# Kernel optimization log

Hardware: AMD Instinct MI355X
Metric: run time of the kernel (lower is better)

The kernel has to match this reference:

```python
import jax, jax.numpy as jnp
import numpy as np

N, K, D = 524288, 32, 8
EPS = 1e-6


def setup_inputs() -> dict:
    key = jax.random.key(0)
    k1, k2, k3, k4 = jax.random.split(key, 4)
    x = jax.random.normal(k1, (N, D), dtype=jnp.float32)
    pi = jax.random.uniform(k2, (K,), dtype=jnp.float32)
    means = jax.random.normal(k3, (K, D), dtype=jnp.float32)
    # eye + small perturbation keeps tril(chol_var) well-conditioned (PD covariance)
    chol_var = jnp.eye(D, dtype=jnp.float32)[None] + 0.1 * jax.random.normal(k4, (K, D, D), dtype=jnp.float32)
    return {"x": x, "pi": pi, "means": means, "chol_var": chol_var}


def reference(x, pi, means, chol_var):
    d = x.shape[-1]
    L = jnp.tril(chol_var)                                   # [K,d,d]
    cov = jnp.einsum('kij,klj->kil', L, L) + EPS * jnp.eye(d, dtype=x.dtype)
    C = jnp.linalg.cholesky(cov)                             # [K,d,d] (MVN recomputes cholesky)
    logdet = 2.0 * jnp.sum(jnp.log(jnp.diagonal(C, axis1=-2, axis2=-1)), axis=-1)  # [K]
    eye = jnp.eye(d, dtype=x.dtype)
    Cinv = jax.vmap(lambda c: jax.scipy.linalg.solve_triangular(c, eye, lower=True))(C)  # [K,d,d]
    zx = jnp.einsum('kij,nj->nki', Cinv, x)                  # [N,K,d]
    zm = jnp.einsum('kij,kj->ki', Cinv, means)               # [K,d]
    maha = jnp.sum((zx - zm[None]) ** 2, axis=-1)            # [N,K]
    log_2pi = jnp.log(2.0 * jnp.pi).astype(x.dtype)
    log_probs = -0.5 * (maha + d * log_2pi + logdet[None])   # [N,K]
    wll = log_probs + jax.nn.log_softmax(pi)[None]
    return jax.scipy.special.logsumexp(wll, axis=1)          # [N]
```

## Files before the change

kernel.cpp:

```cpp
#include <hip/hip_runtime.h>
#include <math.h>

#define K_ 32
#define D_ 8
#define CSTRIDE 48
#define S_ 4

__global__ __launch_bounds__(256) void gmm_fused(
    const float* __restrict__ x,
    const float* __restrict__ pi,
    const float* __restrict__ means,
    const float* __restrict__ chol,
    float* __restrict__ out, int N)
{
    __shared__ float cv[K_ * CSTRIDE];

    const int tid = threadIdx.x;
    if (tid < K_) {
        const int k = tid;

        float L[D_][D_];
#pragma unroll
        for (int i = 0; i < D_; ++i)
#pragma unroll
            for (int j = 0; j <= i; ++j)
                L[i][j] = chol[k * D_ * D_ + i * D_ + j];

        float rd[D_];
#pragma unroll
        for (int i = 0; i < D_; ++i) rd[i] = 1.f / L[i][i];

        float Ci[D_][D_];
#pragma unroll
        for (int j = 0; j < D_; ++j) {
            Ci[j][j] = rd[j];
#pragma unroll
            for (int i = j + 1; i < D_; ++i) {
                float s = 0.f;
#pragma unroll
                for (int m = j; m < i; ++m) s += L[i][m] * Ci[m][j];
                Ci[i][j] = -s * rd[i];
            }
        }

        float logdet = 0.f;
#pragma unroll
        for (int i = 0; i < D_; ++i) logdet += __logf(fabsf(L[i][i]));
        logdet *= 2.f;

        float zm[D_];
#pragma unroll
        for (int i = 0; i < D_; ++i) {
            float s = 0.f;
#pragma unroll
            for (int j = 0; j <= i; ++j) s += Ci[i][j] * means[k * D_ + j];
            zm[i] = s;
        }

        float mx = pi[0];
#pragma unroll
        for (int t = 1; t < K_; ++t) mx = fmaxf(mx, pi[t]);
        float se = 0.f;
#pragma unroll
        for (int t = 0; t < K_; ++t) se += __expf(pi[t] - mx);
        float lse = mx + __logf(se);

        const float LOG2PI = 1.8378770664093453f;
        const float LOG2E  = 1.4426950408889634f;
        const float SQH2   = 0.84932180028801905f;
        float cst2 = ((pi[k] - lse) - 0.5f * (logdet + (float)D_ * LOG2PI)) * LOG2E;

        float* p = cv + k * CSTRIDE;
        int t = 0;
#pragma unroll
        for (int i = 0; i < D_; ++i)
#pragma unroll
            for (int j = 0; j <= i; ++j) p[t++] = Ci[i][j] * SQH2;
#pragma unroll
        for (int i = 0; i < D_; ++i) p[36 + i] = zm[i] * SQH2;
        p[44] = cst2;
        p[45] = 0.f; p[46] = 0.f; p[47] = 0.f;
    }
    __syncthreads();

    const int q = N >> 2;
    const int t = blockIdx.x * 256 + tid;
    if (t >= q) return;

    float xv[S_][D_];
#pragma unroll
    for (int s = 0; s < S_; ++s) {
        const float4* xp = (const float4*)x + (size_t)(t + s * q) * 2;
        float4 a = xp[0], b = xp[1];
        xv[s][0] = a.x; xv[s][1] = a.y; xv[s][2] = a.z; xv[s][3] = a.w;
        xv[s][4] = b.x; xv[s][5] = b.y; xv[s][6] = b.z; xv[s][7] = b.w;
    }

    float m[S_], sm[S_];
#pragma unroll
    for (int s = 0; s < S_; ++s) { m[s] = -INFINITY; sm[s] = 0.f; }

#pragma unroll 1
    for (int k = 0; k < K_; ++k) {
        float c[CSTRIDE];
        {
            const float4* ps = (const float4*)(cv + k * CSTRIDE);
            float4* cd = (float4*)c;
#pragma unroll
            for (int qq = 0; qq < 12; ++qq) cd[qq] = ps[qq];
        }

        float w[S_];
#pragma unroll
        for (int s = 0; s < S_; ++s) w[s] = c[44];
        int tt = 0;
#pragma unroll
        for (int i = 0; i < D_; ++i) {
            float z[S_];
#pragma unroll
            for (int s = 0; s < S_; ++s) z[s] = -c[36 + i];
#pragma unroll
            for (int j = 0; j <= i; ++j)
#pragma unroll
                for (int s = 0; s < S_; ++s)
                    z[s] = fmaf(c[tt + j], xv[s][j], z[s]);
            tt += i + 1;
#pragma unroll
            for (int s = 0; s < S_; ++s) w[s] = fmaf(-z[s], z[s], w[s]);
        }

#pragma unroll
        for (int s = 0; s < S_; ++s) {
            float d = w[s] - m[s];
            float e = exp2f(-fabsf(d));
            sm[s] = (d > 0.f) ? fmaf(sm[s], e, 1.f) : (sm[s] + e);
            m[s] = fmaxf(m[s], w[s]);
        }
    }

    const float LN2 = 0.69314718055994531f;
#pragma unroll
    for (int s = 0; s < S_; ++s)
        out[t + s * q] = (m[s] + log2f(sm[s])) * LN2;
}

extern "C" void kernel_launch(void* const* d_in, const int* in_sizes, int n_in,
                              void* d_out, int out_size, void* d_ws, size_t ws_size,
                              hipStream_t stream) {
    const float* x     = (const float*)d_in[0];
    const float* pi    = (const float*)d_in[1];
    const float* means = (const float*)d_in[2];
    const float* chol  = (const float*)d_in[3];
    float* out = (float*)d_out;

    int N = in_sizes[0] / D_;
    int q = N >> 2;

    gmm_fused<<<(q + 255) / 256, 256, 0, stream>>>(x, pi, means, chol, out, N);
}
```

Before: 88.87 us.

## Recast GMM log-likelihood as fp16 MFMA over quadratic monomial features

The Mahalanobis quadratic form is expanded into a linear function of 44 monomial features (x_i*x_j, x_i, 1) plus a constant. This turns the per-component work into a 32x48 by 48x32 matrix product per tile of 32 points, done with three f16 32x32x16 MFMA instructions per tile instead of scalar FMA triangular solves. The logsumexp drops the running max and sums exp2 directly, and the grid becomes a fixed-size grid-stride loop over tiles. The trade-offs are fp16 rounding of coefficients and squared features, which is exposed to cancellation in the expanded form, and possible exp2 underflow for outlying points because there is no max-shift.

```diff
diff --git a/kernel.cpp b/kernel.cpp
--- a/kernel.cpp
+++ b/kernel.cpp
@@ -3,28 +3,32 @@
 
 #define K_ 32
 #define D_ 8
-#define CSTRIDE 48
-#define S_ 4
+#define NF 48
+#define NTHREADS 256
+#define NBLOCKS 1024
 
-__global__ __launch_bounds__(256) void gmm_fused(
+typedef _Float16 half8 __attribute__((ext_vector_type(8)));
+typedef float f32x16 __attribute__((ext_vector_type(16)));
+
+__global__ __launch_bounds__(NTHREADS) void gmm_mfma(
     const float* __restrict__ x,
     const float* __restrict__ pi,
     const float* __restrict__ means,
     const float* __restrict__ chol,
     float* __restrict__ out, int N)
 {
-    __shared__ float cv[K_ * CSTRIDE];
+    __shared__ __align__(16) _Float16 ldsA[3][64][8];
 
     const int tid = threadIdx.x;
+
     if (tid < K_) {
         const int k = tid;
-
         float L[D_][D_];
 #pragma unroll
         for (int i = 0; i < D_; ++i)
 #pragma unroll
             for (int j = 0; j <= i; ++j)
-                L[i][j] = chol[k * D_ * D_ + i * D_ + j];
+                L[i][j] = chol[k * 64 + i * 8 + j];
 
         float rd[D_];
 #pragma unroll
@@ -48,13 +52,29 @@
         for (int i = 0; i < D_; ++i) logdet += __logf(fabsf(L[i][i]));
         logdet *= 2.f;
 
-        float zm[D_];
+        float A2[D_][D_];
+#pragma unroll
+        for (int i = 0; i < D_; ++i)
+#pragma unroll
+            for (int j = 0; j <= i; ++j) {
+                float s = 0.f;
+#pragma unroll
+                for (int m = i; m < D_; ++m) s += Ci[m][i] * Ci[m][j];
+                A2[i][j] = s;
+                A2[j][i] = s;
+            }
+
+        float mu[D_];
+#pragma unroll
+        for (int j = 0; j < D_; ++j) mu[j] = means[k * 8 + j];
+        float b[D_], q = 0.f;
 #pragma unroll
         for (int i = 0; i < D_; ++i) {
             float s = 0.f;
 #pragma unroll
-            for (int j = 0; j <= i; ++j) s += Ci[i][j] * means[k * D_ + j];
-            zm[i] = s;
+            for (int j = 0; j < D_; ++j) s += A2[i][j] * mu[j];
+            b[i] = s;
+            q += s * mu[i];
         }
 
         float mx = pi[0];
@@ -67,81 +87,84 @@
 
         const float LOG2PI = 1.8378770664093453f;
         const float LOG2E  = 1.4426950408889634f;
-        const float SQH2   = 0.84932180028801905f;
-        float cst2 = ((pi[k] - lse) - 0.5f * (logdet + (float)D_ * LOG2PI)) * LOG2E;
+        const float ALPHA  = 0.72134752044448170f;
+        float cst2 = ((pi[k] - lse) - 0.5f * (logdet + 8.f * LOG2PI)) * LOG2E;
 
-        float* p = cv + k * CSTRIDE;
+        float V[NF];
         int t = 0;
 #pragma unroll
         for (int i = 0; i < D_; ++i)
 #pragma unroll
-            for (int j = 0; j <= i; ++j) p[t++] = Ci[i][j] * SQH2;
+            for (int j = 0; j <= i; ++j)
+                V[t++] = (i == j) ? -ALPHA * A2[i][i] : -2.f * ALPHA * A2[i][j];
 #pragma unroll
-        for (int i = 0; i < D_; ++i) p[36 + i] = zm[i] * SQH2;
-        p[44] = cst2;
-        p[45] = 0.f; p[46] = 0.f; p[47] = 0.f;
+        for (int i = 0; i < D_; ++i) V[36 + i] = 2.f * ALPHA * b[i];
+        V[44] = cst2 - ALPHA * q;
+        V[45] = 0.f; V[46] = 0.f; V[47] = 0.f;
+
+#pragma unroll
+        for (int s = 0; s < 3; ++s)
+#pragma unroll
+            for (int h = 0; h < 2; ++h)
+#pragma unroll
+                for (int j = 0; j < 8; ++j)
+                    ldsA[s][h * 32 + k][j] = (_Float16)V[16 * s + 8 * h + j];
     }
     __syncthreads();
 
-    const int q = N >> 2;
-    const int t = blockIdx.x * 256 + tid;
-    if (t >= q) return;
+    const int lane = tid & 63;
+    const int m    = lane & 31;
+    const bool h1  = lane >= 32;
 
-    float xv[S_][D_];
+    half8 wf[3];
 #pragma unroll
-    for (int s = 0; s < S_; ++s) {
-        const float4* xp = (const float4*)x + (size_t)(t + s * q) * 2;
-        float4 a = xp[0], b = xp[1];
-        xv[s][0] = a.x; xv[s][1] = a.y; xv[s][2] = a.z; xv[s][3] = a.w;
-        xv[s][4] = b.x; xv[s][5] = b.y; xv[s][6] = b.z; xv[s][7] = b.w;
-    }
+    for (int s = 0; s < 3; ++s) wf[s] = *(const half8*)&ldsA[s][lane][0];
 
-    float m[S_], sm[S_];
+    const int ntiles = N >> 5;
+    const int gw = blockIdx.x * (NTHREADS / 64) + (tid >> 6);
+    const int nw = gridDim.x * (NTHREADS / 64);
+    const float4* xp = (const float4*)x;
+    const float LN2 = 0.69314718055994531f;
+
+    for (int tile = gw; tile < ntiles; tile += nw) {
+        const int n = tile * 32 + m;
+        float4 a = xp[2 * n], b2 = xp[2 * n + 1];
+        float xv[D_] = {a.x, a.y, a.z, a.w, b2.x, b2.y, b2.z, b2.w};
+
+        float Y[NF];
+        {
+            int t = 0;
 #pragma unroll
-    for (int s = 0; s < S_; ++s) { m[s] = -INFINITY; sm[s] = 0.f; }
-
-#pragma unroll 1
-    for (int k = 0; k < K_; ++k) {
-        float c[CSTRIDE];
-        {
-            const float4* ps = (const float4*)(cv + k * CSTRIDE);
-            float4* cd = (float4*)c;
+            for (int i = 0; i < D_; ++i)
 #pragma unroll
-            for (int qq = 0; qq < 12; ++qq) cd[qq] = ps[qq];
+                for (int j = 0; j <= i; ++j) Y[t++] = xv[i] * xv[j];
+#pragma unroll
+            for (int i = 0; i < D_; ++i) Y[36 + i] = xv[i];
+            Y[44] = 1.f; Y[45] = 0.f; Y[46] = 0.f; Y[47] = 0.f;
         }
 
-        float w[S_];
+        f32x16 acc;
 #pragma unroll
-        for (int s = 0; s < S_; ++s) w[s] = c[44];
-        int tt = 0;
+        for (int r = 0; r < 16; ++r) acc[r] = 0.f;
+
 #pragma unroll
-        for (int i = 0; i < D_; ++i) {
-            float z[S_];
+        for (int s = 0; s < 3; ++s) {
+            half8 bf;
 #pragma unroll
-            for (int s = 0; s < S_; ++s) z[s] = -c[36 + i];
-#pragma unroll
-            for (int j = 0; j <= i; ++j)
-#pragma unroll
-                for (int s = 0; s < S_; ++s)
-                    z[s] = fmaf(c[tt + j], xv[s][j], z[s]);
-            tt += i + 1;
-#pragma unroll
-            for (int s = 0; s < S_; ++s) w[s] = fmaf(-z[s], z[s], w[s]);
+            for (int j = 0; j < 8; ++j) {
+                float v = h1 ? Y[16 * s + 8 + j] : Y[16 * s + j];
+                bf[j] = (_Float16)v;
+            }
+            acc = __builtin_amdgcn_mfma_f32_32x32x16_f16(wf[s], bf, acc, 0, 0, 0);
         }
 
+        float tot = 0.f;
 #pragma unroll
-        for (int s = 0; s < S_; ++s) {
-            float d = w[s] - m[s];
-            float e = exp2f(-fabsf(d));
-            sm[s] = (d > 0.f) ? fmaf(sm[s], e, 1.f) : (sm[s] + e);
-            m[s] = fmaxf(m[s], w[s]);
-        }
+        for (int r = 0; r < 16; ++r) tot += exp2f(acc[r]);
+        tot += __shfl_xor(tot, 32, 64);
+        float res = log2f(tot) * LN2;
+        if (!h1) out[n] = res;
     }
-
-    const float LN2 = 0.69314718055994531f;
-#pragma unroll
-    for (int s = 0; s < S_; ++s)
-        out[t + s * q] = (m[s] + log2f(sm[s])) * LN2;
 }
 
 extern "C" void kernel_launch(void* const* d_in, const int* in_sizes, int n_in,
@@ -154,7 +177,6 @@
     float* out = (float*)d_out;
 
     int N = in_sizes[0] / D_;
-    int q = N >> 2;
 
-    gmm_fused<<<(q + 255) / 256, 256, 0, stream>>>(x, pi, means, chol, out, N);
+    gmm_mfma<<<NBLOCKS, NTHREADS, 0, stream>>>(x, pi, means, chol, out, N);
 }
```

Result: faster. 77.69 us (-12.6%).
